# Optimization experiments

Hardware: AMD Instinct MI355X
Metric: run time of the kernel (lower is better)

The kernel has to match this reference:

```python
import jax, jax.numpy as jnp
import numpy as np

B, N, K, C = 2, 2048, 48, 128
FF = 4 * C
EPS = 1e-5
SCALE = 30.0

def _gelu(x):
    return jax.nn.gelu(x, approximate=False)

def _ln(x, g, b):
    m = jnp.mean(x, axis=-1, keepdims=True)
    v = jnp.var(x, axis=-1, keepdims=True)
    return g * (x - m) * jax.lax.rsqrt(v + EPS) + b

def _gather_nodes(nodes, idx):
    # nodes [B,N,C], idx [B,N,K] -> [B,N,K,C]
    return jnp.take_along_axis(nodes[:, :, None, :], idx[..., None], axis=1)

def setup_inputs() -> dict:
    key = jax.random.key(0)
    ks = jax.random.split(key, 16)
    def w(k, i, o):
        return (jax.random.normal(k, (i, o), jnp.float32) / np.sqrt(i)).astype(jnp.float32)
    inp = {
        'h_V': jax.random.normal(ks[0], (B, N, C), jnp.float32),
        'h_E': jax.random.normal(ks[1], (B, N, K, C), jnp.float32),
        'E_idx': jax.random.randint(ks[2], (B, N, K), 0, N),
        'mask_V': jnp.ones((B, N), jnp.float32),
        'mask_attend': jnp.ones((B, N, K), jnp.float32),
        'W1_w': w(ks[3], 3 * C, C), 'W1_b': jnp.zeros((C,), jnp.float32),
        'W2_w': w(ks[4], C, C), 'W2_b': jnp.zeros((C,), jnp.float32),
        'W3_w': w(ks[5], C, C), 'W3_b': jnp.zeros((C,), jnp.float32),
        'W11_w': w(ks[6], 3 * C, C), 'W11_b': jnp.zeros((C,), jnp.float32),
        'W12_w': w(ks[7], C, C), 'W12_b': jnp.zeros((C,), jnp.float32),
        'W13_w': w(ks[8], C, C), 'W13_b': jnp.zeros((C,), jnp.float32),
        'Win_w': w(ks[9], C, FF), 'Win_b': jnp.zeros((FF,), jnp.float32),
        'Wout_w': w(ks[10], FF, C), 'Wout_b': jnp.zeros((C,), jnp.float32),
        'g1': jnp.ones((C,), jnp.float32), 'b1': jnp.zeros((C,), jnp.float32),
        'g2': jnp.ones((C,), jnp.float32), 'b2': jnp.zeros((C,), jnp.float32),
        'g3': jnp.ones((C,), jnp.float32), 'b3': jnp.zeros((C,), jnp.float32),
    }
    return inp

def _edge_mlp(h_V, h_E, E_idx, Wa_w, Wa_b, Wb_w, Wb_b, Wc_w, Wc_b):
    h_nbr = _gather_nodes(h_V, E_idx)                       # [B,N,K,C]
    h_ctr = jnp.broadcast_to(h_V[:, :, None, :], h_nbr.shape)
    h_EV = jnp.concatenate([h_ctr, h_E, h_nbr], axis=-1)   # [B,N,K,3C]
    h = _gelu(h_EV @ Wa_w + Wa_b)
    h = _gelu(h @ Wb_w + Wb_b)
    return h @ Wc_w + Wc_b                                  # [B,N,K,C]

def reference(h_V, h_E, E_idx, mask_V, mask_attend,
              W1_w, W1_b, W2_w, W2_b, W3_w, W3_b,
              W11_w, W11_b, W12_w, W12_b, W13_w, W13_b,
              Win_w, Win_b, Wout_w, Wout_b,
              g1, b1, g2, b2, g3, b3):
    # message pass on nodes
    h_msg = _edge_mlp(h_V, h_E, E_idx, W1_w, W1_b, W2_w, W2_b, W3_w, W3_b)
    h_msg = mask_attend[..., None] * h_msg
    dh = jnp.sum(h_msg, axis=-2) / SCALE
    h_V = _ln(h_V + dh, g1, b1)
    # position-wise FFN
    dh = _gelu(h_V @ Win_w + Win_b) @ Wout_w + Wout_b
    h_V = _ln(h_V + dh, g2, b2)
    h_V = mask_V[..., None] * h_V
    # edge update
    h_msg = _edge_mlp(h_V, h_E, E_idx, W11_w, W11_b, W12_w, W12_b, W13_w, W13_b)
    h_E = _ln(h_E + h_msg, g3, b3)
    return (h_V, h_E)
```

## Files before the change

### kernel.cpp

```cpp
#include <hip/hip_runtime.h>
#include <hip/hip_bf16.h>

#define BB 2
#define NN 2048
#define KE 48
#define CC 128
#define FFD 512
#define K3 384

typedef short sx8 __attribute__((ext_vector_type(8)));
typedef float fx4 __attribute__((ext_vector_type(4)));

__device__ __forceinline__ short f2bs(float f) {
    __bf16 h = (__bf16)f;
    return __builtin_bit_cast(short, h);
}

__device__ __forceinline__ float gelu_f(float x) {
    float z = fabsf(x) * 0.70710678118654752f;
    float e = __expf(-z * z);
    float t = __builtin_amdgcn_rcpf(fmaf(0.3275911f, z, 1.0f));
    float poly = t * fmaf(t, fmaf(t, fmaf(t, fmaf(t, 1.061405429f, -1.453152027f),
                                          1.421413741f), -0.284496736f), 0.254829592f);
    float erf = 1.0f - poly * e;
    float phi = fmaf(copysignf(erf, x), 0.5f, 0.5f);
    return x * phi;
}

__device__ __forceinline__ sx8 cvt8f(const float* p) {
    float4 a = *(const float4*)p;
    float4 b = *(const float4*)(p + 4);
    sx8 r;
    r[0] = f2bs(a.x); r[1] = f2bs(a.y); r[2] = f2bs(a.z); r[3] = f2bs(a.w);
    r[4] = f2bs(b.x); r[5] = f2bs(b.y); r[6] = f2bs(b.z); r[7] = f2bs(b.w);
    return r;
}

__global__ void prep_weights(const float* __restrict__ W1, const float* __restrict__ W2,
                             const float* __restrict__ W3, const float* __restrict__ W11,
                             const float* __restrict__ W12, const float* __restrict__ W13,
                             const float* __restrict__ Win, const float* __restrict__ Wout,
                             short* __restrict__ wt) {
    int i = blockIdx.x * 256 + threadIdx.x;
    const float* src;
    short* dst;
    int R, S, local;
    if (i < 49152)       { src = W1;   dst = wt;          R = 384; S = 128; local = i; }
    else if (i < 65536)  { src = W2;   dst = wt + 49152;  R = 128; S = 128; local = i - 49152; }
    else if (i < 81920)  { src = W3;   dst = wt + 65536;  R = 128; S = 128; local = i - 65536; }
    else if (i < 131072) { src = W11;  dst = wt + 81920;  R = 384; S = 128; local = i - 81920; }
    else if (i < 147456) { src = W12;  dst = wt + 131072; R = 128; S = 128; local = i - 131072; }
    else if (i < 163840) { src = W13;  dst = wt + 147456; R = 128; S = 128; local = i - 147456; }
    else if (i < 229376) { src = Win;  dst = wt + 163840; R = 128; S = 512; local = i - 163840; }
    else                 { src = Wout; dst = wt + 229376; R = 512; S = 128; local = i - 229376; }
    int c = local / R;
    int r = local - c * R;
    dst[local] = f2bs(src[r * S + c]);
}

template <int PASS>
__global__ __launch_bounds__(256, 4) void edge_pass(
    const float* __restrict__ hVsrc, const float* __restrict__ hE,
    const int* __restrict__ Eidx,
    const short* __restrict__ WaT, const float* __restrict__ Wab,
    const short* __restrict__ WbT, const float* __restrict__ Wbb,
    const short* __restrict__ WcT, const float* __restrict__ Wcb,
    const float* __restrict__ mask_att, float* __restrict__ hv1_out,
    const float* __restrict__ gamma, const float* __restrict__ beta,
    float* __restrict__ hE_out) {
    __shared__ __align__(16) unsigned char smem_raw[48 * 264 * 2];
    __shared__ __align__(16) short Xs[48 * 136];

    short* A0   = (short*)smem_raw;
    float* S    = (float*)smem_raw;
    float* dhp  = (float*)Xs;
    float* redp = (float*)Xs + 512;

    const int tid = threadIdx.x;
    const int bn  = blockIdx.x;
    const int bb  = bn >> 11;
    const int wave = tid >> 6, lane = tid & 63, q = lane >> 4, m16 = lane & 15;
    const int col0 = wave * 32 + m16;
    const int col1 = col0 + 16;
    const int r0 = tid >> 4, seg = tid & 15;

    const int e0 = Eidx[bn * KE + r0];
    const int e1 = Eidx[bn * KE + r0 + 16];
    const int e2 = Eidx[bn * KE + r0 + 32];

    const float* ctr = hVsrc + (size_t)bn * CC;
    sx8 cA[4], s0f[4], s1f[4];
#pragma unroll
    for (int kk = 0; kk < 4; ++kk) {
        cA[kk]  = cvt8f(ctr + kk * 32 + q * 8);
        s0f[kk] = *(const sx8*)(WaT + col0 * K3 + kk * 32 + q * 8);
        s1f[kk] = *(const sx8*)(WaT + col1 * K3 + kk * 32 + q * 8);
    }

    {
        const float* he = hE + (size_t)bn * KE * CC + seg * 8;
        *(sx8*)(A0 + r0 * 264 + seg * 8)        = cvt8f(he + r0 * CC);
        *(sx8*)(A0 + (r0 + 16) * 264 + seg * 8) = cvt8f(he + (r0 + 16) * CC);
        *(sx8*)(A0 + (r0 + 32) * 264 + seg * 8) = cvt8f(he + (r0 + 32) * CC);
        const float* hvb = hVsrc + (size_t)bb * NN * CC + seg * 8;
        *(sx8*)(A0 + r0 * 264 + 128 + seg * 8)        = cvt8f(hvb + (size_t)e0 * CC);
        *(sx8*)(A0 + (r0 + 16) * 264 + 128 + seg * 8) = cvt8f(hvb + (size_t)e1 * CC);
        *(sx8*)(A0 + (r0 + 32) * 264 + 128 + seg * 8) = cvt8f(hvb + (size_t)e2 * CC);
    }

    fx4 acc[3][2];
    {
        fx4 c0, c1;
#pragma unroll
        for (int r = 0; r < 4; ++r) { c0[r] = 0.0f; c1[r] = 0.0f; }
#pragma unroll
        for (int kk = 0; kk < 4; ++kk) {
            c0 = __builtin_amdgcn_mfma_f32_16x16x32_bf16(cA[kk], s0f[kk], c0, 0, 0, 0);
            c1 = __builtin_amdgcn_mfma_f32_16x16x32_bf16(cA[kk], s1f[kk], c1, 0, 0, 0);
        }
#pragma unroll
        for (int mt = 0; mt < 3; ++mt) { acc[mt][0] = c0; acc[mt][1] = c1; }
    }

    sx8 b0[4], b1[4];
#pragma unroll
    for (int kk = 0; kk < 4; ++kk) {
        b0[kk] = *(const sx8*)(WaT + col0 * K3 + 128 + kk * 32 + q * 8);
        b1[kk] = *(const sx8*)(WaT + col1 * K3 + 128 + kk * 32 + q * 8);
    }
    __syncthreads();

#pragma unroll
    for (int half = 0; half < 2; ++half) {
        if (half) {
#pragma unroll
            for (int kk = 0; kk < 4; ++kk) {
                b0[kk] = *(const sx8*)(WaT + col0 * K3 + 256 + kk * 32 + q * 8);
                b1[kk] = *(const sx8*)(WaT + col1 * K3 + 256 + kk * 32 + q * 8);
            }
        }
#pragma unroll
        for (int kk = 0; kk < 4; ++kk) {
#pragma unroll
            for (int mt = 0; mt < 3; ++mt) {
                sx8 af = *(const sx8*)(A0 + (mt * 16 + m16) * 264 + half * 128 + kk * 32 + q * 8);
                acc[mt][0] = __builtin_amdgcn_mfma_f32_16x16x32_bf16(af, b0[kk], acc[mt][0], 0, 0, 0);
                acc[mt][1] = __builtin_amdgcn_mfma_f32_16x16x32_bf16(af, b1[kk], acc[mt][1], 0, 0, 0);
            }
        }
    }

    sx8 p0[4], p1[4];
#pragma unroll
    for (int kk = 0; kk < 4; ++kk) {
        p0[kk] = *(const sx8*)(WbT + col0 * CC + kk * 32 + q * 8);
        p1[kk] = *(const sx8*)(WbT + col1 * CC + kk * 32 + q * 8);
    }

    {
        float ba0 = Wab[col0], ba1 = Wab[col1];
#pragma unroll
        for (int mt = 0; mt < 3; ++mt)
#pragma unroll
            for (int r = 0; r < 4; ++r) {
                int row = mt * 16 + q * 4 + r;
                Xs[row * 136 + col0] = f2bs(gelu_f(acc[mt][0][r] + ba0));
                Xs[row * 136 + col1] = f2bs(gelu_f(acc[mt][1][r] + ba1));
            }
    }
    __syncthreads();

    fx4 acc2[3][2];
#pragma unroll
    for (int mt = 0; mt < 3; ++mt)
#pragma unroll
        for (int nt = 0; nt < 2; ++nt)
#pragma unroll
            for (int r = 0; r < 4; ++r) acc2[mt][nt][r] = 0.0f;
#pragma unroll
    for (int kk = 0; kk < 4; ++kk) {
#pragma unroll
        for (int mt = 0; mt < 3; ++mt) {
            sx8 af = *(const sx8*)(Xs + (mt * 16 + m16) * 136 + kk * 32 + q * 8);
            acc2[mt][0] = __builtin_amdgcn_mfma_f32_16x16x32_bf16(af, p0[kk], acc2[mt][0], 0, 0, 0);
            acc2[mt][1] = __builtin_amdgcn_mfma_f32_16x16x32_bf16(af, p1[kk], acc2[mt][1], 0, 0, 0);
        }
    }

    sx8 t0[4], t1[4];
#pragma unroll
    for (int kk = 0; kk < 4; ++kk) {
        t0[kk] = *(const sx8*)(WcT + col0 * CC + kk * 32 + q * 8);
        t1[kk] = *(const sx8*)(WcT + col1 * CC + kk * 32 + q * 8);
    }
    float mrow[12];
    float res0[12], res1[12];
    if constexpr (PASS == 1) {
#pragma unroll
        for (int mt = 0; mt < 3; ++mt)
#pragma unroll
            for (int r = 0; r < 4; ++r)
                mrow[mt * 4 + r] = mask_att[bn * KE + mt * 16 + q * 4 + r];
    } else {
#pragma unroll
        for (int mt = 0; mt < 3; ++mt)
#pragma unroll
            for (int r = 0; r < 4; ++r) {
                int row = mt * 16 + q * 4 + r;
                res0[mt * 4 + r] = hE[((size_t)bn * KE + row) * CC + col0];
                res1[mt * 4 + r] = hE[((size_t)bn * KE + row) * CC + col1];
            }
    }
    __syncthreads();

    {
        float bb0 = Wbb[col0], bb1 = Wbb[col1];
#pragma unroll
        for (int mt = 0; mt < 3; ++mt)
#pragma unroll
            for (int r = 0; r < 4; ++r) {
                int row = mt * 16 + q * 4 + r;
                Xs[row * 136 + col0] = f2bs(gelu_f(acc2[mt][0][r] + bb0));
                Xs[row * 136 + col1] = f2bs(gelu_f(acc2[mt][1][r] + bb1));
            }
    }
    __syncthreads();

    fx4 acc3[3][2];
#pragma unroll
    for (int mt = 0; mt < 3; ++mt)
#pragma unroll
        for (int nt = 0; nt < 2; ++nt)
#pragma unroll
            for (int r = 0; r < 4; ++r) acc3[mt][nt][r] = 0.0f;
#pragma unroll
    for (int kk = 0; kk < 4; ++kk) {
#pragma unroll
        for (int mt = 0; mt < 3; ++mt) {
            sx8 af = *(const sx8*)(Xs + (mt * 16 + m16) * 136 + kk * 32 + q * 8);
            acc3[mt][0] = __builtin_amdgcn_mfma_f32_16x16x32_bf16(af, t0[kk], acc3[mt][0], 0, 0, 0);
            acc3[mt][1] = __builtin_amdgcn_mfma_f32_16x16x32_bf16(af, t1[kk], acc3[mt][1], 0, 0, 0);
        }
    }

    float bc0 = Wcb[col0], bc1 = Wcb[col1];

    if constexpr (PASS == 1) {
        float ps0 = 0.f, ps1 = 0.f;
#pragma unroll
        for (int mt = 0; mt < 3; ++mt)
#pragma unroll
            for (int r = 0; r < 4; ++r) {
                float m = mrow[mt * 4 + r];
                ps0 += m * (acc3[mt][0][r] + bc0);
                ps1 += m * (acc3[mt][1][r] + bc1);
            }
        __syncthreads();
        dhp[q * 128 + col0] = ps0;
        dhp[q * 128 + col1] = ps1;
        __syncthreads();
        float val = 0.f;
        if (tid < 128) {
            float dh = dhp[tid] + dhp[128 + tid] + dhp[256 + tid] + dhp[384 + tid];
            val = hVsrc[(size_t)bn * CC + tid] + dh * (1.0f / 30.0f);
            float sv1 = val, sv2 = val * val;
#pragma unroll
            for (int m = 32; m >= 1; m >>= 1) {
                sv1 += __shfl_xor(sv1, m);
                sv2 += __shfl_xor(sv2, m);
            }
            if ((tid & 63) == 0) {
                redp[(tid >> 6) * 2]     = sv1;
                redp[(tid >> 6) * 2 + 1] = sv2;
            }
        }
        __syncthreads();
        if (tid < 128) {
            float mean = (redp[0] + redp[2]) * (1.0f / 128.0f);
            float var  = (redp[1] + redp[3]) * (1.0f / 128.0f) - mean * mean;
            float rstd = rsqrtf(fmaxf(var, 0.0f) + 1e-5f);
            hv1_out[(size_t)bn * CC + tid] = gamma[tid] * (val - mean) * rstd + beta[tid];
        }
    } else {
#pragma unroll
        for (int mt = 0; mt < 3; ++mt)
#pragma unroll
            for (int r = 0; r < 4; ++r) {
                int row = mt * 16 + q * 4 + r;
                S[row * 132 + col0] = res0[mt * 4 + r] + acc3[mt][0][r] + bc0;
                S[row * 132 + col1] = res1[mt * 4 + r] + acc3[mt][1][r] + bc1;
            }
        __syncthreads();
        int g = tid >> 5, l32 = tid & 31;
        for (int r = g; r < 48; r += 8) {
            float x0 = S[r * 132 + l32];
            float x1 = S[r * 132 + l32 + 32];
            float x2 = S[r * 132 + l32 + 64];
            float x3 = S[r * 132 + l32 + 96];
            float sv1 = x0 + x1 + x2 + x3;
            float sv2 = x0 * x0 + x1 * x1 + x2 * x2 + x3 * x3;
#pragma unroll
            for (int m = 16; m >= 1; m >>= 1) {
                sv1 += __shfl_xor(sv1, m, 32);
                sv2 += __shfl_xor(sv2, m, 32);
            }
            float mean = sv1 * (1.0f / 128.0f);
            float var  = sv2 * (1.0f / 128.0f) - mean * mean;
            float rstd = rsqrtf(fmaxf(var, 0.0f) + 1e-5f);
            float* orow = hE_out + ((size_t)bn * KE + r) * CC;
            orow[l32]      = gamma[l32] * (x0 - mean) * rstd + beta[l32];
            orow[l32 + 32] = gamma[l32 + 32] * (x1 - mean) * rstd + beta[l32 + 32];
            orow[l32 + 64] = gamma[l32 + 64] * (x2 - mean) * rstd + beta[l32 + 64];
            orow[l32 + 96] = gamma[l32 + 96] * (x3 - mean) * rstd + beta[l32 + 96];
        }
    }
}

__global__ __launch_bounds__(256) void ffn_kernel(
    float* __restrict__ hv, const short* __restrict__ WinT,
    const float* __restrict__ Winb, const short* __restrict__ WoutT,
    const float* __restrict__ Woutb, const float* __restrict__ g2,
    const float* __restrict__ b2, const float* __restrict__ maskV) {
    __shared__ __align__(16) float hvF[16 * 132];
    __shared__ __align__(16) short Abf[16 * 136];
    __shared__ __align__(16) short Xs[16 * 520];

    const int tid = threadIdx.x;
    const int bn  = blockIdx.x;
    const int wave = tid >> 6, lane = tid & 63, q = lane >> 4, m16 = lane & 15;

    for (int i = tid; i < 512; i += 256) {
        int row = i >> 5;
        int c4  = (i & 31) * 4;
        float4 v = *(const float4*)(hv + (bn * 16 + row) * CC + c4);
        hvF[row * 132 + c4]     = v.x;
        hvF[row * 132 + c4 + 1] = v.y;
        hvF[row * 132 + c4 + 2] = v.z;
        hvF[row * 132 + c4 + 3] = v.w;
        Abf[row * 136 + c4]     = f2bs(v.x);
        Abf[row * 136 + c4 + 1] = f2bs(v.y);
        Abf[row * 136 + c4 + 2] = f2bs(v.z);
        Abf[row * 136 + c4 + 3] = f2bs(v.w);
    }
    __syncthreads();

    fx4 acc1[8];
#pragma unroll
    for (int nt = 0; nt < 8; ++nt)
#pragma unroll
        for (int r = 0; r < 4; ++r) acc1[nt][r] = 0.0f;

#pragma unroll
    for (int kk = 0; kk < 4; ++kk) {
        sx8 af = *(const sx8*)(Abf + m16 * 136 + kk * 32 + q * 8);
#pragma unroll
        for (int nt = 0; nt < 8; ++nt) {
            int coln = wave * 128 + nt * 16 + m16;
            sx8 bf = *(const sx8*)(WinT + coln * CC + kk * 32 + q * 8);
            acc1[nt] = __builtin_amdgcn_mfma_f32_16x16x32_bf16(af, bf, acc1[nt], 0, 0, 0);
        }
    }
#pragma unroll
    for (int nt = 0; nt < 8; ++nt) {
        int coln = wave * 128 + nt * 16 + m16;
        float bi = Winb[coln];
#pragma unroll
        for (int r = 0; r < 4; ++r) {
            int row = q * 4 + r;
            Xs[row * 520 + coln] = f2bs(gelu_f(acc1[nt][r] + bi));
        }
    }
    __syncthreads();

    const int col0 = wave * 32 + m16, col1 = col0 + 16;
    fx4 o0, o1;
#pragma unroll
    for (int r = 0; r < 4; ++r) { o0[r] = 0.0f; o1[r] = 0.0f; }
#pragma unroll
    for (int kk = 0; kk < 16; ++kk) {
        sx8 af = *(const sx8*)(Xs + m16 * 520 + kk * 32 + q * 8);
        sx8 b0 = *(const sx8*)(WoutT + col0 * FFD + kk * 32 + q * 8);
        sx8 b1 = *(const sx8*)(WoutT + col1 * FFD + kk * 32 + q * 8);
        o0 = __builtin_amdgcn_mfma_f32_16x16x32_bf16(af, b0, o0, 0, 0, 0);
        o1 = __builtin_amdgcn_mfma_f32_16x16x32_bf16(af, b1, o1, 0, 0, 0);
    }
    {
        float bo0 = Woutb[col0], bo1 = Woutb[col1];
#pragma unroll
        for (int r = 0; r < 4; ++r) {
            int row = q * 4 + r;
            hvF[row * 132 + col0] += o0[r] + bo0;
            hvF[row * 132 + col1] += o1[r] + bo1;
        }
    }
    __syncthreads();

    int g = tid >> 5, l32 = tid & 31;
#pragma unroll
    for (int rr = 0; rr < 2; ++rr) {
        int row = g + rr * 8;
        float x0 = hvF[row * 132 + l32];
        float x1 = hvF[row * 132 + l32 + 32];
        float x2 = hvF[row * 132 + l32 + 64];
        float x3 = hvF[row * 132 + l32 + 96];
        float s1 = x0 + x1 + x2 + x3;
        float s2 = x0 * x0 + x1 * x1 + x2 * x2 + x3 * x3;
#pragma unroll
        for (int m = 16; m >= 1; m >>= 1) {
            s1 += __shfl_xor(s1, m, 32);
            s2 += __shfl_xor(s2, m, 32);
        }
        float mean = s1 * (1.0f / 128.0f);
        float var  = s2 * (1.0f / 128.0f) - mean * mean;
        float rstd = rsqrtf(fmaxf(var, 0.0f) + 1e-5f);
        int node = bn * 16 + row;
        float mk = maskV[node];
        float* orow = hv + node * CC;
        orow[l32]      = mk * (g2[l32] * (x0 - mean) * rstd + b2[l32]);
        orow[l32 + 32] = mk * (g2[l32 + 32] * (x1 - mean) * rstd + b2[l32 + 32]);
        orow[l32 + 64] = mk * (g2[l32 + 64] * (x2 - mean) * rstd + b2[l32 + 64]);
        orow[l32 + 96] = mk * (g2[l32 + 96] * (x3 - mean) * rstd + b2[l32 + 96]);
    }
}

extern "C" void kernel_launch(void* const* d_in, const int* in_sizes, int n_in,
                              void* d_out, int out_size, void* d_ws, size_t ws_size,
                              hipStream_t stream) {
    (void)in_sizes; (void)n_in; (void)out_size; (void)ws_size;
    const float* hV    = (const float*)d_in[0];
    const float* hE    = (const float*)d_in[1];
    const int*   Eidx  = (const int*)d_in[2];
    const float* maskV = (const float*)d_in[3];
    const float* maskA = (const float*)d_in[4];
    const float* W1w  = (const float*)d_in[5];
    const float* W1b  = (const float*)d_in[6];
    const float* W2w  = (const float*)d_in[7];
    const float* W2b  = (const float*)d_in[8];
    const float* W3w  = (const float*)d_in[9];
    const float* W3b  = (const float*)d_in[10];
    const float* W11w = (const float*)d_in[11];
    const float* W11b = (const float*)d_in[12];
    const float* W12w = (const float*)d_in[13];
    const float* W12b = (const float*)d_in[14];
    const float* W13w = (const float*)d_in[15];
    const float* W13b = (const float*)d_in[16];
    const float* Winw = (const float*)d_in[17];
    const float* Winb = (const float*)d_in[18];
    const float* Woutw = (const float*)d_in[19];
    const float* Woutb = (const float*)d_in[20];
    const float* g1 = (const float*)d_in[21];
    const float* b1 = (const float*)d_in[22];
    const float* g2 = (const float*)d_in[23];
    const float* b2 = (const float*)d_in[24];
    const float* g3 = (const float*)d_in[25];
    const float* b3 = (const float*)d_in[26];

    short* wt   = (short*)d_ws;
    float* outV = (float*)d_out;
    float* outE = outV + (size_t)BB * NN * CC;

    prep_weights<<<1152, 256, 0, stream>>>(W1w, W2w, W3w, W11w, W12w, W13w, Winw, Woutw, wt);
    edge_pass<1><<<BB * NN, 256, 0, stream>>>(hV, hE, Eidx,
                                              wt, W1b, wt + 49152, W2b, wt + 65536, W3b,
                                              maskA, outV, g1, b1, nullptr);
    ffn_kernel<<<256, 256, 0, stream>>>(outV, wt + 163840, Winb, wt + 229376, Woutb, g2, b2, maskV);
    edge_pass<2><<<BB * NN, 256, 0, stream>>>(outV, hE, Eidx,
                                              wt + 81920, W11b, wt + 131072, W12b, wt + 147456, W13b,
                                              nullptr, nullptr, g3, b3, outE);
}
```

Baseline: 407.2 us.

## Alias edge-pass LDS buffers, raise occupancy, and prefetch FFN weights into registers

The edge pass now aliases the GELU activation buffer Xs and the reduction scratch onto the single A0 shared-memory region, which cuts LDS per block, and raises the launch-bounds occupancy hint from 4 to 6 blocks per CU. Barriers are moved so the aliased buffer is not overwritten while still being read. Global loads for h_E and gathered neighbours are issued together before conversion to expose more memory-level parallelism. In the FFN kernel all Win and Wout weight fragments are loaded into registers up front so global latency overlaps other work, at the cost of heavy register pressure and possible spills.

Result: slower. 424.2 us (+4.2%).

```diff
diff --git a/kernel.cpp b/kernel.cpp
--- a/kernel.cpp
+++ b/kernel.cpp
@@ -30,6 +30,13 @@
 __device__ __forceinline__ sx8 cvt8f(const float* p) {
     float4 a = *(const float4*)p;
     float4 b = *(const float4*)(p + 4);
+    sx8 r;
+    r[0] = f2bs(a.x); r[1] = f2bs(a.y); r[2] = f2bs(a.z); r[3] = f2bs(a.w);
+    r[4] = f2bs(b.x); r[5] = f2bs(b.y); r[6] = f2bs(b.z); r[7] = f2bs(b.w);
+    return r;
+}
+
+__device__ __forceinline__ sx8 pack8(float4 a, float4 b) {
     sx8 r;
     r[0] = f2bs(a.x); r[1] = f2bs(a.y); r[2] = f2bs(a.z); r[3] = f2bs(a.w);
     r[4] = f2bs(b.x); r[5] = f2bs(b.y); r[6] = f2bs(b.z); r[7] = f2bs(b.w);
@@ -59,7 +66,7 @@
 }
 
 template <int PASS>
-__global__ __launch_bounds__(256, 4) void edge_pass(
+__global__ __launch_bounds__(256, 6) void edge_pass(
     const float* __restrict__ hVsrc, const float* __restrict__ hE,
     const int* __restrict__ Eidx,
     const short* __restrict__ WaT, const float* __restrict__ Wab,
@@ -69,12 +76,12 @@
     const float* __restrict__ gamma, const float* __restrict__ beta,
     float* __restrict__ hE_out) {
     __shared__ __align__(16) unsigned char smem_raw[48 * 264 * 2];
-    __shared__ __align__(16) short Xs[48 * 136];
 
     short* A0   = (short*)smem_raw;
+    short* Xs   = (short*)smem_raw;
     float* S    = (float*)smem_raw;
-    float* dhp  = (float*)Xs;
-    float* redp = (float*)Xs + 512;
+    float* dhp  = (float*)(smem_raw + 13056);
+    float* redp = (float*)(smem_raw + 15104);
 
     const int tid = threadIdx.x;
     const int bn  = blockIdx.x;
@@ -88,28 +95,39 @@
     const int e1 = Eidx[bn * KE + r0 + 16];
     const int e2 = Eidx[bn * KE + r0 + 32];
 
+    {
+        const float* he  = hE + (size_t)bn * KE * CC + seg * 8;
+        const float* hvb = hVsrc + (size_t)bb * NN * CC + seg * 8;
+        float4 h0a = *(const float4*)(he + r0 * CC);
+        float4 h0b = *(const float4*)(he + r0 * CC + 4);
+        float4 h1a = *(const float4*)(he + (r0 + 16) * CC);
+        float4 h1b = *(const float4*)(he + (r0 + 16) * CC + 4);
+        float4 h2a = *(const float4*)(he + (r0 + 32) * CC);
+        float4 h2b = *(const float4*)(he + (r0 + 32) * CC + 4);
+        float4 n0a = *(const float4*)(hvb + (size_t)e0 * CC);
+        float4 n0b = *(const float4*)(hvb + (size_t)e0 * CC + 4);
+        float4 n1a = *(const float4*)(hvb + (size_t)e1 * CC);
+        float4 n1b = *(const float4*)(hvb + (size_t)e1 * CC + 4);
+        float4 n2a = *(const float4*)(hvb + (size_t)e2 * CC);
+        float4 n2b = *(const float4*)(hvb + (size_t)e2 * CC + 4);
+        *(sx8*)(A0 + r0 * 264 + seg * 8)              = pack8(h0a, h0b);
+        *(sx8*)(A0 + (r0 + 16) * 264 + seg * 8)       = pack8(h1a, h1b);
+        *(sx8*)(A0 + (r0 + 32) * 264 + seg * 8)       = pack8(h2a, h2b);
+        *(sx8*)(A0 + r0 * 264 + 128 + seg * 8)        = pack8(n0a, n0b);
+        *(sx8*)(A0 + (r0 + 16) * 264 + 128 + seg * 8) = pack8(n1a, n1b);
+        *(sx8*)(A0 + (r0 + 32) * 264 + 128 + seg * 8) = pack8(n2a, n2b);
+    }
+
     const float* ctr = hVsrc + (size_t)bn * CC;
-    sx8 cA[4], s0f[4], s1f[4];
-#pragma unroll
-    for (int kk = 0; kk < 4; ++kk) {
-        cA[kk]  = cvt8f(ctr + kk * 32 + q * 8);
-        s0f[kk] = *(const sx8*)(WaT + col0 * K3 + kk * 32 + q * 8);
-        s1f[kk] = *(const sx8*)(WaT + col1 * K3 + kk * 32 + q * 8);
-    }
-
-    {
-        const float* he = hE + (size_t)bn * KE * CC + seg * 8;
-        *(sx8*)(A0 + r0 * 264 + seg * 8)        = cvt8f(he + r0 * CC);
-        *(sx8*)(A0 + (r0 + 16) * 264 + seg * 8) = cvt8f(he + (r0 + 16) * CC);
-        *(sx8*)(A0 + (r0 + 32) * 264 + seg * 8) = cvt8f(he + (r0 + 32) * CC);
-        const float* hvb = hVsrc + (size_t)bb * NN * CC + seg * 8;
-        *(sx8*)(A0 + r0 * 264 + 128 + seg * 8)        = cvt8f(hvb + (size_t)e0 * CC);
-        *(sx8*)(A0 + (r0 + 16) * 264 + 128 + seg * 8) = cvt8f(hvb + (size_t)e1 * CC);
-        *(sx8*)(A0 + (r0 + 32) * 264 + 128 + seg * 8) = cvt8f(hvb + (size_t)e2 * CC);
-    }
-
     fx4 acc[3][2];
     {
+        sx8 cA[4], s0f[4], s1f[4];
+#pragma unroll
+        for (int kk = 0; kk < 4; ++kk) {
+            cA[kk]  = cvt8f(ctr + kk * 32 + q * 8);
+            s0f[kk] = *(const sx8*)(WaT + col0 * K3 + kk * 32 + q * 8);
+            s1f[kk] = *(const sx8*)(WaT + col1 * K3 + kk * 32 + q * 8);
+        }
         fx4 c0, c1;
 #pragma unroll
         for (int r = 0; r < 4; ++r) { c0[r] = 0.0f; c1[r] = 0.0f; }
@@ -156,6 +174,7 @@
         p0[kk] = *(const sx8*)(WbT + col0 * CC + kk * 32 + q * 8);
         p1[kk] = *(const sx8*)(WbT + col1 * CC + kk * 32 + q * 8);
     }
+    __syncthreads();
 
     {
         float ba0 = Wab[col0], ba1 = Wab[col1];
@@ -255,7 +274,6 @@
                 ps0 += m * (acc3[mt][0][r] + bc0);
                 ps1 += m * (acc3[mt][1][r] + bc1);
             }
-        __syncthreads();
         dhp[q * 128 + col0] = ps0;
         dhp[q * 128 + col1] = ps1;
         __syncthreads();
@@ -282,6 +300,7 @@
             hv1_out[(size_t)bn * CC + tid] = gamma[tid] * (val - mean) * rstd + beta[tid];
         }
     } else {
+        __syncthreads();
 #pragma unroll
         for (int mt = 0; mt < 3; ++mt)
 #pragma unroll
@@ -316,7 +335,7 @@
     }
 }
 
-__global__ __launch_bounds__(256) void ffn_kernel(
+__global__ __launch_bounds__(256, 1) void ffn_kernel(
     float* __restrict__ hv, const short* __restrict__ WinT,
     const float* __restrict__ Winb, const short* __restrict__ WoutT,
     const float* __restrict__ Woutb, const float* __restrict__ g2,
@@ -328,6 +347,14 @@
     const int tid = threadIdx.x;
     const int bn  = blockIdx.x;
     const int wave = tid >> 6, lane = tid & 63, q = lane >> 4, m16 = lane & 15;
+    const int col0 = wave * 32 + m16, col1 = col0 + 16;
+
+    sx8 bw[4][8];
+#pragma unroll
+    for (int kk = 0; kk < 4; ++kk)
+#pragma unroll
+        for (int nt = 0; nt < 8; ++nt)
+            bw[kk][nt] = *(const sx8*)(WinT + (wave * 128 + nt * 16 + m16) * CC + kk * 32 + q * 8);
 
     for (int i = tid; i < 512; i += 256) {
         int row = i >> 5;
@@ -354,12 +381,17 @@
     for (int kk = 0; kk < 4; ++kk) {
         sx8 af = *(const sx8*)(Abf + m16 * 136 + kk * 32 + q * 8);
 #pragma unroll
-        for (int nt = 0; nt < 8; ++nt) {
-            int coln = wave * 128 + nt * 16 + m16;
-            sx8 bf = *(const sx8*)(WinT + coln * CC + kk * 32 + q * 8);
-            acc1[nt] = __builtin_amdgcn_mfma_f32_16x16x32_bf16(af, bf, acc1[nt], 0, 0, 0);
-        }
-    }
+        for (int nt = 0; nt < 8; ++nt)
+            acc1[nt] = __builtin_amdgcn_mfma_f32_16x16x32_bf16(af, bw[kk][nt], acc1[nt], 0, 0, 0);
+    }
+
+    sx8 c0a[16], c1a[16];
+#pragma unroll
+    for (int kk = 0; kk < 16; ++kk) {
+        c0a[kk] = *(const sx8*)(WoutT + col0 * FFD + kk * 32 + q * 8);
+        c1a[kk] = *(const sx8*)(WoutT + col1 * FFD + kk * 32 + q * 8);
+    }
+
 #pragma unroll
     for (int nt = 0; nt < 8; ++nt) {
         int coln = wave * 128 + nt * 16 + m16;
@@ -372,17 +404,14 @@
     }
     __syncthreads();
 
-    const int col0 = wave * 32 + m16, col1 = col0 + 16;
     fx4 o0, o1;
 #pragma unroll
     for (int r = 0; r < 4; ++r) { o0[r] = 0.0f; o1[r] = 0.0f; }
 #pragma unroll
     for (int kk = 0; kk < 16; ++kk) {
         sx8 af = *(const sx8*)(Xs + m16 * 520 + kk * 32 + q * 8);
-        sx8 b0 = *(const sx8*)(WoutT + col0 * FFD + kk * 32 + q * 8);
-        sx8 b1 = *(const sx8*)(WoutT + col1 * FFD + kk * 32 + q * 8);
-        o0 = __builtin_amdgcn_mfma_f32_16x16x32_bf16(af, b0, o0, 0, 0, 0);
-        o1 = __builtin_amdgcn_mfma_f32_16x16x32_bf16(af, b1, o1, 0, 0, 0);
+        o0 = __builtin_amdgcn_mfma_f32_16x16x32_bf16(af, c0a[kk], o0, 0, 0, 0);
+        o1 = __builtin_amdgcn_mfma_f32_16x16x32_bf16(af, c1a[kk], o1, 0, 0, 0);
     }
     {
         float bo0 = Woutb[col0], bo1 = Woutb[col1];
```
